# Kernel optimization log

Hardware: AMD Instinct MI355X
Metric: run time of the kernel (lower is better)

Reference implementation:

```python
import jax, jax.numpy as jnp
import numpy as np

DIM = 33
EPS = 1e-5

def _conv(x, w, b, stride, pad):
    y = jax.lax.conv_general_dilated(x, w, (stride, stride), [(pad, pad), (pad, pad)],
                                     dimension_numbers=('NCHW', 'OIHW', 'NCHW'))
    return y + b[None, :, None, None]

def _lrelu(x):
    return jnp.where(x >= 0, x, 0.2 * x)

def _inorm(x, g, b):
    m = x.mean(axis=(2, 3), keepdims=True)
    v = x.var(axis=(2, 3), keepdims=True)
    return (x - m) * jax.lax.rsqrt(v + EPS) * g[None, :, None, None] + b[None, :, None, None]

def _classifier(img, w1, b1, g1, be1, w2, b2, g2, be2, w3, b3, g3, be3,
                w4, b4, g4, be4, w5, b5, w6, b6):
    x = jax.image.resize(img, (img.shape[0], 3, 256, 256), method='bilinear')
    x = _inorm(_lrelu(_conv(x, w1, b1, 2, 1)), g1, be1)   # [B,16,128,128]
    x = _inorm(_lrelu(_conv(x, w2, b2, 2, 1)), g2, be2)   # [B,32,64,64]
    x = _inorm(_lrelu(_conv(x, w3, b3, 2, 1)), g3, be3)   # [B,64,32,32]
    x = _inorm(_lrelu(_conv(x, w4, b4, 2, 1)), g4, be4)   # [B,128,16,16]
    x = _lrelu(_conv(x, w5, b5, 2, 1))                     # [B,128,8,8]
    x = _conv(x, w6, b6, 1, 0)                             # [B,3,1,1]
    return x.reshape(-1)                                   # squeeze (B=1) -> [3]

def _trilinear(lut, img):
    # lut: [3, dim, dim, dim] indexed [c, b_idx, g_idx, r_idx]; img: [B,3,H,W] in [0,1]
    scale = DIM - 1
    x = img * scale
    idx = jnp.clip(jnp.floor(x), 0, DIM - 2).astype(jnp.int32)
    f = x - idx                                            # fractional weights (differentiable in img)
    ir, ig, ib = idx[:, 0], idx[:, 1], idx[:, 2]           # [B,H,W]
    fr, fg, fb = f[:, 0], f[:, 1], f[:, 2]
    out = jnp.zeros((3,) + ir.shape, dtype=img.dtype)
    for db in (0, 1):
        wb = fb if db else 1.0 - fb
        for dg in (0, 1):
            wg = fg if dg else 1.0 - fg
            for dr in (0, 1):
                wr = fr if dr else 1.0 - fr
                corner = lut[:, ib + db, ig + dg, ir + dr]  # [3,B,H,W] gather
                out = out + (wb * wg * wr)[None] * corner
    return jnp.transpose(out, (1, 0, 2, 3))                # [B,3,H,W]

def _forward(image_input, lut0, lut1, lut2, w1, b1, g1, be1, w2, b2, g2, be2,
             w3, b3, g3, be3, w4, b4, g4, be4, w5, b5, w6, b6):
    pred = _classifier(image_input, w1, b1, g1, be1, w2, b2, g2, be2, w3, b3, g3, be3,
                       w4, b4, g4, be4, w5, b5, w6, b6)
    final_lut = pred[0] * lut0 + pred[1] * lut1 + pred[2] * lut2
    return _trilinear(final_lut, image_input)

def setup_inputs() -> dict:
    key = jax.random.key(0)
    ks = jax.random.split(key, 16)
    B, H, W = 1, 2160, 3840
    d = {}
    d['image_input'] = jax.random.uniform(ks[0], (B, 3, H, W), dtype=jnp.float32)
    d['lut0'] = jax.random.normal(ks[1], (3, DIM, DIM, DIM), dtype=jnp.float32)
    d['lut1'] = jax.random.normal(ks[2], (3, DIM, DIM, DIM), dtype=jnp.float32)
    d['lut2'] = jax.random.normal(ks[3], (3, DIM, DIM, DIM), dtype=jnp.float32)
    s = 0.05
    d['w1'] = jax.random.normal(ks[4], (16, 3, 3, 3), dtype=jnp.float32) * s
    d['b1'] = jnp.zeros((16,), jnp.float32); d['g1'] = jnp.ones((16,), jnp.float32); d['be1'] = jnp.zeros((16,), jnp.float32)
    d['w2'] = jax.random.normal(ks[5], (32, 16, 3, 3), dtype=jnp.float32) * s
    d['b2'] = jnp.zeros((32,), jnp.float32); d['g2'] = jnp.ones((32,), jnp.float32); d['be2'] = jnp.zeros((32,), jnp.float32)
    d['w3'] = jax.random.normal(ks[6], (64, 32, 3, 3), dtype=jnp.float32) * s
    d['b3'] = jnp.zeros((64,), jnp.float32); d['g3'] = jnp.ones((64,), jnp.float32); d['be3'] = jnp.zeros((64,), jnp.float32)
    d['w4'] = jax.random.normal(ks[7], (128, 64, 3, 3), dtype=jnp.float32) * s
    d['b4'] = jnp.zeros((128,), jnp.float32); d['g4'] = jnp.ones((128,), jnp.float32); d['be4'] = jnp.zeros((128,), jnp.float32)
    d['w5'] = jax.random.normal(ks[8], (128, 128, 3, 3), dtype=jnp.float32) * s
    d['b5'] = jnp.zeros((128,), jnp.float32)
    d['w6'] = jax.random.normal(ks[9], (3, 128, 8, 8), dtype=jnp.float32) * s
    d['b6'] = jnp.zeros((3,), jnp.float32)
    return d

def reference(image_input, lut0, lut1, lut2, w1, b1, g1, be1, w2, b2, g2, be2,
              w3, b3, g3, be3, w4, b4, g4, be4, w5, b5, w6, b6):
    return _forward(image_input, lut0, lut1, lut2, w1, b1, g1, be1, w2, b2, g2, be2,
                    w3, b3, g3, be3, w4, b4, g4, be4, w5, b5, w6, b6)
```

## Files before the change

### kernel.cpp

```cpp
#include <hip/hip_runtime.h>

#define NPX (2160*3840)
#define EPS 1e-5f

typedef float __attribute__((ext_vector_type(4))) fx4;

__global__ __launch_bounds__(256) void resize_w_kernel(const float* __restrict__ img,
                                                       float* __restrict__ tmp) {
  __shared__ __align__(16) float row[3872];
  const int bh = blockIdx.x;
  const float* src = img + (size_t)bh * 3840;
  const int tid = threadIdx.x;
  if (tid < 16) { row[tid] = 0.f; row[3856 + tid] = 0.f; }
  const float4* s4 = (const float4*)src;
  float4* r4 = (float4*)(row + 16);
  for (int i = tid; i < 960; i += 256) r4[i] = s4[i];
  __syncthreads();
  const int i = tid;
  const float* rp = row + 15*i + 9;
  float acc = 0.f;
  #pragma unroll
  for (int k = 0; k < 29; ++k) {
    const float w = (float)(15 - (k < 14 ? 14 - k : k - 14));
    acc = fmaf(w, rp[k], acc);
  }
  const float rcpw = (i == 0 || i == 255) ? (1.f/197.f) : (1.f/225.f);
  tmp[bh*256 + i] = acc * rcpw;
}

__global__ __launch_bounds__(256) void resize_h_kernel(const float* __restrict__ tmp,
                                                       float* __restrict__ dst) {
  const int c = blockIdx.x >> 8;
  const int oh = blockIdx.x & 255;
  const int ow = threadIdx.x;
  const float sf = ((float)oh + 0.5f) * 8.4375f - 0.5f;
  int lo = (int)ceilf(sf - 8.4375f); if (lo < 0) lo = 0;
  int hi = (int)floorf(sf + 8.4375f); if (hi > 2159) hi = 2159;
  float acc = 0.f, wsum = 0.f;
  for (int j = lo; j <= hi; ++j) {
    const float w = 1.f - fabsf(sf - (float)j) * (16.f/135.f);
    acc = fmaf(w, tmp[(c*2160 + j)*256 + ow], acc);
    wsum += w;
  }
  dst[blockIdx.x*256 + ow] = acc / wsum;
}

template<int CIN,int CICHUNK,int HIN,int WIN,int HOUT,int WOUT,int TH,int NPIN,int MODE>
__global__ __launch_bounds__(256) void conv_fused(
    const float* __restrict__ in, const float* __restrict__ wt, const float* __restrict__ bias,
    const float* __restrict__ pin, const float* __restrict__ gin, const float* __restrict__ bin,
    float* __restrict__ out, float* __restrict__ pout,
    const float* __restrict__ gself, const float* __restrict__ bself) {
  constexpr int NTW = WOUT/16;
  constexpr int NT  = (HOUT/TH)*NTW;
  constexpr int NCHUNK = CIN/CICHUNK;
  constexpr int HROWS = 2*TH + 1;
  constexpr int SLOTS = CICHUNK*HROWS*9;
  constexpr float PHW_INV = 1.f/(float)(HIN*WIN);

  __shared__ float sx[CICHUNK*HROWS*36];
  __shared__ float wl[CIN*9];
  __shared__ float sA[CIN], sB[CIN];
  __shared__ float2 wred[4];

  const int co = blockIdx.x / NT;
  const int t  = blockIdx.x % NT;
  const int oh0 = (t / NTW)*TH, ow0 = (t % NTW)*16;
  const int tid = threadIdx.x;

  for (int i = tid; i < CIN*9; i += 256) wl[i] = wt[co*CIN*9 + i];
  if (NPIN > 0) {
    if (tid < CIN) {
      const float2* p2 = (const float2*)pin;
      float s = 0.f, q = 0.f;
      #pragma unroll 4
      for (int k = 0; k < NPIN; ++k) { float2 p = p2[tid*NPIN + k]; s += p.x; q += p.y; }
      const float m = s * PHW_INV;
      float var = q * PHW_INV - m*m; var = fmaxf(var, 0.f);
      const float A = gin[tid] * rsqrtf(var + EPS);
      sA[tid] = A; sB[tid] = bin[tid] - m*A;
    }
  }
  __syncthreads();

  const int ohl = tid >> 4, owl = tid & 15;
  const bool active = (ohl < TH);
  float acc = bias[co];

  for (int cc = 0; cc < NCHUNK; ++cc) {
    if (cc) __syncthreads();
    const int cb = cc*CICHUNK;
    for (int i = tid; i < SLOTS; i += 256) {
      const int ci_l = i / (HROWS*9);
      const int rem  = i - ci_l*(HROWS*9);
      const int r = rem / 9, q = rem - r*9;
      const int grow = 2*oh0 - 1 + r;
      const int ga   = 2*ow0 - 4 + 4*q;
      float4 v = make_float4(0.f,0.f,0.f,0.f);
      if (grow >= 0 && grow < HIN && ga >= 0) {
        v = *(const float4*)(in + ((size_t)(cb+ci_l)*HIN + grow)*WIN + ga);
        if (NPIN > 0) {
          const float A = sA[cb+ci_l], B = sB[cb+ci_l];
          v.x = fmaf(A, v.x, B); v.y = fmaf(A, v.y, B);
          v.z = fmaf(A, v.z, B); v.w = fmaf(A, v.w, B);
        }
      }
      *(float4*)&sx[(ci_l*HROWS + r)*36 + q*4] = v;
    }
    __syncthreads();
    if (active) {
      #pragma unroll 4
      for (int ci_l = 0; ci_l < CICHUNK; ++ci_l) {
        const float* sp = sx + ci_l*(HROWS*36);
        const float* wp = wl + (cb+ci_l)*9;
        #pragma unroll
        for (int kh = 0; kh < 3; ++kh) {
          const float* rp = sp + (2*ohl + kh)*36 + 3 + 2*owl;
          acc = fmaf(rp[0], wp[kh*3+0], acc);
          acc = fmaf(rp[1], wp[kh*3+1], acc);
          acc = fmaf(rp[2], wp[kh*3+2], acc);
        }
      }
    }
  }

  acc = acc >= 0.f ? acc : 0.2f*acc;
  if (active) out[(size_t)co*HOUT*WOUT + (oh0+ohl)*WOUT + ow0 + owl] = acc;

  float s = active ? acc : 0.f;
  float q = active ? acc*acc : 0.f;
  #pragma unroll
  for (int off = 32; off > 0; off >>= 1) {
    s += __shfl_down(s, off);
    q += __shfl_down(q, off);
  }
  if ((tid & 63) == 0) wred[tid >> 6] = make_float2(s, q);
  __syncthreads();
  if (tid == 0) {
    const float S = wred[0].x + wred[1].x + wred[2].x + wred[3].x;
    const float Q = wred[0].y + wred[1].y + wred[2].y + wred[3].y;
    if (MODE == 1) {
      ((float2*)pout)[co*NT + t] = make_float2(S, Q);
    } else {
      const float m = S / (float)(HOUT*WOUT);
      float var = Q / (float)(HOUT*WOUT) - m*m; var = fmaxf(var, 0.f);
      const float A = gself[co] * rsqrtf(var + EPS);
      pout[co*2]   = A;
      pout[co*2+1] = bself[co] - m*A;
    }
  }
}

__global__ __launch_bounds__(256) void conv5_fused(const float* __restrict__ in,
    const float* __restrict__ wt, const float* __restrict__ bias,
    const float* __restrict__ pin, const float* __restrict__ gin, const float* __restrict__ bin,
    const float* __restrict__ w6, float* __restrict__ part) {
  __shared__ float sx[32*17*20];
  __shared__ float wl[128*9];
  __shared__ float sA[128], sB[128];
  __shared__ float red[256];
  const int co = blockIdx.x;
  const int tid = threadIdx.x;
  for (int i = tid; i < 1152; i += 256) wl[i] = wt[co*1152 + i];
  if (tid < 128) {
    const float2* p2 = (const float2*)pin;
    const float2 pa = p2[tid*2], pb = p2[tid*2+1];
    const float m = (pa.x + pb.x) * (1.f/256.f);
    float var = (pa.y + pb.y) * (1.f/256.f) - m*m; var = fmaxf(var, 0.f);
    const float A = gin[tid] * rsqrtf(var + EPS);
    sA[tid] = A; sB[tid] = bin[tid] - m*A;
  }
  __syncthreads();

  const int px = tid & 63, q = tid >> 6;
  const int ohl = px >> 3, owl = px & 7;
  float acc = 0.f;
  for (int cc = 0; cc < 4; ++cc) {
    if (cc) __syncthreads();
    const int cb = cc*32;
    for (int i = tid; i < 32*17*5; i += 256) {
      const int ci_l = i / 85;
      const int rem  = i - ci_l*85;
      const int r = rem / 5, qq = rem - r*5;
      const int grow = r - 1;
      const int ga   = 4*qq - 4;
      float4 v = make_float4(0.f,0.f,0.f,0.f);
      if (grow >= 0 && grow < 16 && ga >= 0) {
        v = *(const float4*)(in + ((size_t)(cb+ci_l)*16 + grow)*16 + ga);
        const float A = sA[cb+ci_l], B = sB[cb+ci_l];
        v.x = fmaf(A, v.x, B); v.y = fmaf(A, v.y, B);
        v.z = fmaf(A, v.z, B); v.w = fmaf(A, v.w, B);
      }
      *(float4*)&sx[(ci_l*17 + r)*20 + qq*4] = v;
    }
    __syncthreads();
    #pragma unroll 2
    for (int k = 0; k < 8; ++k) {
      const int ci_l = q*8 + k;
      const float* sp = sx + ci_l*340;
      const float* wp = wl + (cb+ci_l)*9;
      #pragma unroll
      for (int kh = 0; kh < 3; ++kh) {
        const float* rp = sp + (2*ohl + kh)*20 + 3 + 2*owl;
        acc = fmaf(rp[0], wp[kh*3+0], acc);
        acc = fmaf(rp[1], wp[kh*3+1], acc);
        acc = fmaf(rp[2], wp[kh*3+2], acc);
      }
    }
  }
  red[tid] = acc;
  __syncthreads();
  if (tid < 64) {
    float a = red[tid] + red[tid+64] + red[tid+128] + red[tid+192] + bias[co];
    a = a >= 0.f ? a : 0.2f*a;
    #pragma unroll
    for (int j = 0; j < 3; ++j) {
      float v = a * w6[(j*128 + co)*64 + tid];
      #pragma unroll
      for (int off = 32; off > 0; off >>= 1) v += __shfl_down(v, off);
      if (tid == 0) part[co*3 + j] = v;
    }
  }
}

__global__ __launch_bounds__(256) void blend_pack_kernel(const float* __restrict__ l0,
    const float* __restrict__ l1, const float* __restrict__ l2,
    const float* __restrict__ part, const float* __restrict__ b6,
    unsigned* __restrict__ flp) {
  __shared__ float sred[2][3];
  __shared__ float sp[3];
  const int tid = threadIdx.x;
  float a0 = 0.f, a1 = 0.f, a2 = 0.f;
  if (tid < 128) { a0 = part[tid*3]; a1 = part[tid*3+1]; a2 = part[tid*3+2]; }
  #pragma unroll
  for (int off = 32; off > 0; off >>= 1) {
    a0 += __shfl_down(a0, off);
    a1 += __shfl_down(a1, off);
    a2 += __shfl_down(a2, off);
  }
  if (tid < 128 && (tid & 63) == 0) {
    sred[tid >> 6][0] = a0; sred[tid >> 6][1] = a1; sred[tid >> 6][2] = a2;
  }
  __syncthreads();
  if (tid < 3) sp[tid] = sred[0][tid] + sred[1][tid] + b6[tid];
  __syncthreads();
  const int i = blockIdx.x*256 + tid;
  if (i >= 3*18513) return;
  const int c = i / 18513, rem = i - c*18513;
  const int row = rem / 17, j = rem - row*17;
  const int src = c*35937 + row*33 + 2*j;
  const float v0 = sp[0]*l0[src] + sp[1]*l1[src] + sp[2]*l2[src];
  float v1 = 0.f;
  if (2*j + 1 <= 32) v1 = sp[0]*l0[src+1] + sp[1]*l1[src+1] + sp[2]*l2[src+1];
  unsigned u0 = __float_as_uint(v0); u0 = (u0 + 0x7fffu + ((u0>>16)&1u)) >> 16;
  unsigned u1 = __float_as_uint(v1); u1 = (u1 + 0x7fffu + ((u1>>16)&1u)) >> 16;
  flp[c*18516 + rem] = u0 | (u1 << 16);
}

__global__ __launch_bounds__(1024, 8) void trilinear_kernel(const float* __restrict__ img,
    const unsigned* __restrict__ flp, float* __restrict__ out) {
  __shared__ unsigned slut[18516];
  const int tid = threadIdx.x;
  const int b = blockIdx.x;
  const int x = b & 7;
  const int j = b >> 3;
  const int chunk = x*32 + j/3;
  const int c     = j % 3;
  {
    uint4* d4 = (uint4*)slut;
    const uint4* s4 = (const uint4*)(flp + c*18516);
    for (int i = tid; i < 4629; i += 1024) d4[i] = s4[i];
  }
  __syncthreads();
  const int p0 = chunk * 32400;
  const float* imR = img + p0;
  const float* imG = img + NPX + p0;
  const float* imB = img + 2*NPX + p0;
  float* op = out + (size_t)c*NPX + p0;
  for (int g = tid; g < 4050; g += 1024) {
    const int pA = 4*g;
    const int pB = pA + 16200;
    float rv[8], gv[8], bv[8], ov[8];
    {
      const float4 A = *(const float4*)(imR + pA);
      const float4 B = *(const float4*)(imR + pB);
      rv[0]=A.x; rv[1]=A.y; rv[2]=A.z; rv[3]=A.w;
      rv[4]=B.x; rv[5]=B.y; rv[6]=B.z; rv[7]=B.w;
    }
    {
      const float4 A = *(const float4*)(imG + pA);
      const float4 B = *(const float4*)(imG + pB);
      gv[0]=A.x; gv[1]=A.y; gv[2]=A.z; gv[3]=A.w;
      gv[4]=B.x; gv[5]=B.y; gv[6]=B.z; gv[7]=B.w;
    }
    {
      const float4 A = *(const float4*)(imB + pA);
      const float4 B = *(const float4*)(imB + pB);
      bv[0]=A.x; bv[1]=A.y; bv[2]=A.z; bv[3]=A.w;
      bv[4]=B.x; bv[5]=B.y; bv[6]=B.z; bv[7]=B.w;
    }
    #pragma unroll
    for (int k = 0; k < 8; ++k) {
      const float xr = rv[k]*32.f, xg = gv[k]*32.f, xb = bv[k]*32.f;
      const int ir = (int)xr, ig = (int)xg, ib = (int)xb;
      const float fr = xr - (float)ir;
      const float fg = xg - (float)ig;
      const float fb = xb - (float)ib;
      const int rb = (ib*33 + ig)*17;
      const int jA = rb + (ir >> 1);
      const int jB = rb + ((ir + 1) >> 1);
      const unsigned sh = (ir & 1) * 16;
      const unsigned w0a = slut[jA],       w0b = slut[jB];
      const unsigned w1a = slut[jA + 17],  w1b = slut[jB + 17];
      const unsigned w2a = slut[jA + 561], w2b = slut[jB + 561];
      const unsigned w3a = slut[jA + 578], w3b = slut[jB + 578];
      const unsigned r0 = __builtin_amdgcn_alignbit(w0b, w0a, sh);
      const unsigned r1 = __builtin_amdgcn_alignbit(w1b, w1a, sh);
      const unsigned r2 = __builtin_amdgcn_alignbit(w2b, w2a, sh);
      const unsigned r3 = __builtin_amdgcn_alignbit(w3b, w3a, sh);
      const float v000 = __uint_as_float(r0 << 16), v001 = __uint_as_float(r0 & 0xffff0000u);
      const float v010 = __uint_as_float(r1 << 16), v011 = __uint_as_float(r1 & 0xffff0000u);
      const float v100 = __uint_as_float(r2 << 16), v101 = __uint_as_float(r2 & 0xffff0000u);
      const float v110 = __uint_as_float(r3 << 16), v111 = __uint_as_float(r3 & 0xffff0000u);
      const float a0 = fmaf(fr, v001 - v000, v000);
      const float a1 = fmaf(fr, v011 - v010, v010);
      const float a2 = fmaf(fr, v101 - v100, v100);
      const float a3 = fmaf(fr, v111 - v110, v110);
      const float lo = fmaf(fg, a1 - a0, a0);
      const float hi = fmaf(fg, a3 - a2, a2);
      ov[k] = fmaf(fb, hi - lo, lo);
    }
    fx4 r0 = {ov[0], ov[1], ov[2], ov[3]};
    fx4 r1 = {ov[4], ov[5], ov[6], ov[7]};
    __builtin_nontemporal_store(r0, (fx4*)(op + pA));
    __builtin_nontemporal_store(r1, (fx4*)(op + pB));
  }
}

extern "C" void kernel_launch(void* const* d_in, const int* in_sizes, int n_in,
                              void* d_out, int out_size, void* d_ws, size_t ws_size,
                              hipStream_t stream) {
  const float* img  = (const float*)d_in[0];
  const float* lut0 = (const float*)d_in[1];
  const float* lut1 = (const float*)d_in[2];
  const float* lut2 = (const float*)d_in[3];
  const float* w1 = (const float*)d_in[4];  const float* b1  = (const float*)d_in[5];
  const float* g1 = (const float*)d_in[6];  const float* be1 = (const float*)d_in[7];
  const float* w2 = (const float*)d_in[8];  const float* b2  = (const float*)d_in[9];
  const float* g2 = (const float*)d_in[10]; const float* be2 = (const float*)d_in[11];
  const float* w3 = (const float*)d_in[12]; const float* b3  = (const float*)d_in[13];
  const float* g3 = (const float*)d_in[14]; const float* be3 = (const float*)d_in[15];
  const float* w4 = (const float*)d_in[16]; const float* b4  = (const float*)d_in[17];
  const float* g4 = (const float*)d_in[18]; const float* be4 = (const float*)d_in[19];
  const float* w5 = (const float*)d_in[20]; const float* b5  = (const float*)d_in[21];
  const float* w6 = (const float*)d_in[22]; const float* b6  = (const float*)d_in[23];

  float* ws = (float*)d_ws;
  float* tmp   = ws;
  float* r256  = ws + 1658880;
  float* c1    = ws;
  float* c2    = ws + 262144;
  float* c3    = ws + 393216;
  float* c4    = ws + 458752;
  float* part1 = ws + 491520;
  float* part2 = ws + 493568;
  float* part3 = ws + 494592;
  float* part4 = ws + 495104;
  float* part6 = ws + 495616;
  unsigned* flp = (unsigned*)(ws + 496128);

  resize_w_kernel<<<3*2160, 256, 0, stream>>>(img, tmp);
  resize_h_kernel<<<3*256, 256, 0, stream>>>(tmp, r256);

  conv_fused< 3, 3,256,256,128,128,16, 0,1><<<16*64, 256, 0, stream>>>(
      r256, w1, b1, nullptr, nullptr, nullptr, c1, part1, nullptr, nullptr);
  conv_fused<16,16,128,128, 64, 64,16,64,1><<<32*16, 256, 0, stream>>>(
      c1, w2, b2, part1, g1, be1, c2, part2, nullptr, nullptr);
  conv_fused<32,32, 64, 64, 32, 32,16,16,1><<<64*4, 256, 0, stream>>>(
      c2, w3, b3, part2, g2, be2, c3, part3, nullptr, nullptr);
  conv_fused<64,32, 32, 32, 16, 16, 8, 4,1><<<128*2, 256, 0, stream>>>(
      c3, w4, b4, part3, g3, be3, c4, part4, nullptr, nullptr);
  conv5_fused<<<128, 256, 0, stream>>>(c4, w5, b5, part4, g4, be4, w6, part6);

  blend_pack_kernel<<<218, 256, 0, stream>>>(lut0, lut1, lut2, part6, b6, flp);
  trilinear_kernel<<<768, 1024, 0, stream>>>(img, flp, (float*)d_out);
}
```

Measured before the change: 165.1 us.

## Fuse conv tail and LUT blend into one cooperative kernel with grid syncs

Merges the five classifier conv stages and the LUT blend/pack kernel into a single cooperative kernel of 256 blocks that loops over work units and uses grid-wide syncs between stages. This removes five kernel launch gaps and their drain/fill bubbles. Stages 3 and 4 now use a smaller input-channel chunk of 16, and all stages share one statically sized shared-memory buffer. The cost is grid-sync overhead, the large shared allocation limiting occupancy, and serial looping for the bigger first stages.

```diff
diff --git a/kernel.cpp b/kernel.cpp
--- a/kernel.cpp
+++ b/kernel.cpp
@@ -1,4 +1,7 @@
 #include <hip/hip_runtime.h>
+#include <hip/hip_cooperative_groups.h>
+
+namespace cg = cooperative_groups;
 
 #define NPX (2160*3840)
 #define EPS 1e-5f
@@ -45,28 +48,28 @@
   dst[blockIdx.x*256 + ow] = acc / wsum;
 }
 
-template<int CIN,int CICHUNK,int HIN,int WIN,int HOUT,int WOUT,int TH,int NPIN,int MODE>
-__global__ __launch_bounds__(256) void conv_fused(
+template<int CIN,int CICHUNK,int HIN,int WIN,int HOUT,int WOUT,int TH,int NPIN>
+__device__ __forceinline__ void conv_stage(int unit, int tid, float* smem,
     const float* __restrict__ in, const float* __restrict__ wt, const float* __restrict__ bias,
     const float* __restrict__ pin, const float* __restrict__ gin, const float* __restrict__ bin,
-    float* __restrict__ out, float* __restrict__ pout,
-    const float* __restrict__ gself, const float* __restrict__ bself) {
+    float* __restrict__ out, float2* __restrict__ pout) {
   constexpr int NTW = WOUT/16;
   constexpr int NT  = (HOUT/TH)*NTW;
   constexpr int NCHUNK = CIN/CICHUNK;
   constexpr int HROWS = 2*TH + 1;
   constexpr int SLOTS = CICHUNK*HROWS*9;
   constexpr float PHW_INV = 1.f/(float)(HIN*WIN);
-
-  __shared__ float sx[CICHUNK*HROWS*36];
-  __shared__ float wl[CIN*9];
-  __shared__ float sA[CIN], sB[CIN];
-  __shared__ float2 wred[4];
-
-  const int co = blockIdx.x / NT;
-  const int t  = blockIdx.x % NT;
+  constexpr int WOFF = (CICHUNK*HROWS*36 + CIN*9 + 2*CIN + 1) & ~1;
+
+  float* sx = smem;
+  float* wl = smem + CICHUNK*HROWS*36;
+  float* sA = wl + CIN*9;
+  float* sB = sA + CIN;
+  float2* wred = (float2*)(smem + WOFF);
+
+  const int co = unit / NT;
+  const int t  = unit % NT;
   const int oh0 = (t / NTW)*TH, ow0 = (t % NTW)*16;
-  const int tid = threadIdx.x;
 
   for (int i = tid; i < CIN*9; i += 256) wl[i] = wt[co*CIN*9 + i];
   if (NPIN > 0) {
@@ -139,28 +142,19 @@
   if (tid == 0) {
     const float S = wred[0].x + wred[1].x + wred[2].x + wred[3].x;
     const float Q = wred[0].y + wred[1].y + wred[2].y + wred[3].y;
-    if (MODE == 1) {
-      ((float2*)pout)[co*NT + t] = make_float2(S, Q);
-    } else {
-      const float m = S / (float)(HOUT*WOUT);
-      float var = Q / (float)(HOUT*WOUT) - m*m; var = fmaxf(var, 0.f);
-      const float A = gself[co] * rsqrtf(var + EPS);
-      pout[co*2]   = A;
-      pout[co*2+1] = bself[co] - m*A;
-    }
-  }
-}
-
-__global__ __launch_bounds__(256) void conv5_fused(const float* __restrict__ in,
-    const float* __restrict__ wt, const float* __restrict__ bias,
+    pout[co*NT + t] = make_float2(S, Q);
+  }
+}
+
+__device__ __forceinline__ void conv5_stage(int co, int tid, float* smem,
+    const float* __restrict__ in, const float* __restrict__ wt, const float* __restrict__ bias,
     const float* __restrict__ pin, const float* __restrict__ gin, const float* __restrict__ bin,
     const float* __restrict__ w6, float* __restrict__ part) {
-  __shared__ float sx[32*17*20];
-  __shared__ float wl[128*9];
-  __shared__ float sA[128], sB[128];
-  __shared__ float red[256];
-  const int co = blockIdx.x;
-  const int tid = threadIdx.x;
+  float* sx  = smem;
+  float* wl  = smem + 10880;
+  float* sA  = smem + 12032;
+  float* sB  = smem + 12160;
+  float* red = smem + 12288;
   for (int i = tid; i < 1152; i += 256) wl[i] = wt[co*1152 + i];
   if (tid < 128) {
     const float2* p2 = (const float2*)pin;
@@ -223,13 +217,12 @@
   }
 }
 
-__global__ __launch_bounds__(256) void blend_pack_kernel(const float* __restrict__ l0,
-    const float* __restrict__ l1, const float* __restrict__ l2,
+__device__ __forceinline__ void bp_stage(int b, int tid, float* smem,
+    const float* __restrict__ l0, const float* __restrict__ l1, const float* __restrict__ l2,
     const float* __restrict__ part, const float* __restrict__ b6,
     unsigned* __restrict__ flp) {
-  __shared__ float sred[2][3];
-  __shared__ float sp[3];
-  const int tid = threadIdx.x;
+  float* sp   = smem;
+  float* sred = smem + 4;
   float a0 = 0.f, a1 = 0.f, a2 = 0.f;
   if (tid < 128) { a0 = part[tid*3]; a1 = part[tid*3+1]; a2 = part[tid*3+2]; }
   #pragma unroll
@@ -239,12 +232,12 @@
     a2 += __shfl_down(a2, off);
   }
   if (tid < 128 && (tid & 63) == 0) {
-    sred[tid >> 6][0] = a0; sred[tid >> 6][1] = a1; sred[tid >> 6][2] = a2;
-  }
-  __syncthreads();
-  if (tid < 3) sp[tid] = sred[0][tid] + sred[1][tid] + b6[tid];
-  __syncthreads();
-  const int i = blockIdx.x*256 + tid;
+    sred[(tid >> 6)*3 + 0] = a0; sred[(tid >> 6)*3 + 1] = a1; sred[(tid >> 6)*3 + 2] = a2;
+  }
+  __syncthreads();
+  if (tid < 3) sp[tid] = sred[tid] + sred[3 + tid] + b6[tid];
+  __syncthreads();
+  const int i = b*256 + tid;
   if (i >= 3*18513) return;
   const int c = i / 18513, rem = i - c*18513;
   const int row = rem / 17, j = rem - row*17;
@@ -255,6 +248,49 @@
   unsigned u0 = __float_as_uint(v0); u0 = (u0 + 0x7fffu + ((u0>>16)&1u)) >> 16;
   unsigned u1 = __float_as_uint(v1); u1 = (u1 + 0x7fffu + ((u1>>16)&1u)) >> 16;
   flp[c*18516 + rem] = u0 | (u1 << 16);
+}
+
+struct TailArgs {
+  const float *r256, *w1, *b1;
+  const float *w2, *b2, *g1, *be1;
+  const float *w3, *b3, *g2, *be2;
+  const float *w4, *b4, *g3, *be3;
+  const float *w5, *b5, *g4, *be4;
+  const float *w6, *b6;
+  const float *l0, *l1, *l2;
+  float *c1, *c2, *c3, *c4;
+  float *part1, *part2, *part3, *part4, *part6;
+  unsigned *flp;
+};
+
+__global__ __launch_bounds__(256) void tail_fused(TailArgs a) {
+  __shared__ __align__(16) float smem[19376];
+  cg::grid_group grid = cg::this_grid();
+  const int b = blockIdx.x;
+  const int tid = threadIdx.x;
+
+  for (int u = b; u < 1024; u += 256) {
+    conv_stage<3,3,256,256,128,128,16,0>(u, tid, smem, a.r256, a.w1, a.b1,
+        nullptr, nullptr, nullptr, a.c1, (float2*)a.part1);
+    __syncthreads();
+  }
+  grid.sync();
+  for (int u = b; u < 512; u += 256) {
+    conv_stage<16,16,128,128,64,64,16,64>(u, tid, smem, a.c1, a.w2, a.b2,
+        a.part1, a.g1, a.be1, a.c2, (float2*)a.part2);
+    __syncthreads();
+  }
+  grid.sync();
+  conv_stage<32,16,64,64,32,32,16,16>(b, tid, smem, a.c2, a.w3, a.b3,
+      a.part2, a.g2, a.be2, a.c3, (float2*)a.part3);
+  grid.sync();
+  conv_stage<64,16,32,32,16,16,8,4>(b, tid, smem, a.c3, a.w4, a.b4,
+      a.part3, a.g3, a.be3, a.c4, (float2*)a.part4);
+  grid.sync();
+  if (b < 128)
+    conv5_stage(b, tid, smem, a.c4, a.w5, a.b5, a.part4, a.g4, a.be4, a.w6, a.part6);
+  grid.sync();
+  bp_stage(b, tid, smem, a.l0, a.l1, a.l2, a.part6, a.b6, a.flp);
 }
 
 __global__ __launch_bounds__(1024, 8) void trilinear_kernel(const float* __restrict__ img,
@@ -372,16 +408,19 @@
   resize_w_kernel<<<3*2160, 256, 0, stream>>>(img, tmp);
   resize_h_kernel<<<3*256, 256, 0, stream>>>(tmp, r256);
 
-  conv_fused< 3, 3,256,256,128,128,16, 0,1><<<16*64, 256, 0, stream>>>(
-      r256, w1, b1, nullptr, nullptr, nullptr, c1, part1, nullptr, nullptr);
-  conv_fused<16,16,128,128, 64, 64,16,64,1><<<32*16, 256, 0, stream>>>(
-      c1, w2, b2, part1, g1, be1, c2, part2, nullptr, nullptr);
-  conv_fused<32,32, 64, 64, 32, 32,16,16,1><<<64*4, 256, 0, stream>>>(
-      c2, w3, b3, part2, g2, be2, c3, part3, nullptr, nullptr);
-  conv_fused<64,32, 32, 32, 16, 16, 8, 4,1><<<128*2, 256, 0, stream>>>(
-      c3, w4, b4, part3, g3, be3, c4, part4, nullptr, nullptr);
-  conv5_fused<<<128, 256, 0, stream>>>(c4, w5, b5, part4, g4, be4, w6, part6);
-
-  blend_pack_kernel<<<218, 256, 0, stream>>>(lut0, lut1, lut2, part6, b6, flp);
+  TailArgs ta;
+  ta.r256 = r256; ta.w1 = w1; ta.b1 = b1;
+  ta.w2 = w2; ta.b2 = b2; ta.g1 = g1; ta.be1 = be1;
+  ta.w3 = w3; ta.b3 = b3; ta.g2 = g2; ta.be2 = be2;
+  ta.w4 = w4; ta.b4 = b4; ta.g3 = g3; ta.be3 = be3;
+  ta.w5 = w5; ta.b5 = b5; ta.g4 = g4; ta.be4 = be4;
+  ta.w6 = w6; ta.b6 = b6;
+  ta.l0 = lut0; ta.l1 = lut1; ta.l2 = lut2;
+  ta.c1 = c1; ta.c2 = c2; ta.c3 = c3; ta.c4 = c4;
+  ta.part1 = part1; ta.part2 = part2; ta.part3 = part3; ta.part4 = part4; ta.part6 = part6;
+  ta.flp = flp;
+  void* kargs[] = { (void*)&ta };
+  hipLaunchCooperativeKernel(tail_fused, dim3(256), dim3(256), kargs, 0, stream);
+
   trilinear_kernel<<<768, 1024, 0, stream>>>(img, flp, (float*)d_out);
 }
```

After: 308.9 us. 87.1% more time.
